# Kernel tuning notes

Measured on AMD Instinct MI355X. Metric: run time of the kernel, lower is better.

The kernel has to match this reference:

```python
import jax, jax.numpy as jnp
import numpy as np

N_EMBD = 1024
N_HEADS = 16
HEAD_DIM = N_EMBD // N_HEADS


def setup_inputs() -> dict:
    key = jax.random.key(0)
    ks = jax.random.split(key, 5)
    s = 0.02
    return {
        "x": jax.random.normal(ks[0], (4, 2048, N_EMBD), dtype=jnp.float32),
        "w_attn": jax.random.normal(ks[1], (N_EMBD, 3 * N_EMBD), dtype=jnp.float32) * s,
        "b_attn": jnp.zeros((3 * N_EMBD,), dtype=jnp.float32),
        "w_proj": jax.random.normal(ks[2], (N_EMBD, N_EMBD), dtype=jnp.float32) * s,
        "b_proj": jnp.zeros((N_EMBD,), dtype=jnp.float32),
    }


def reference(x, w_attn, b_attn, w_proj, b_proj):
    B, T, C = x.shape
    H, D = N_HEADS, HEAD_DIM
    qkv = x @ w_attn + b_attn                      # [B,T,3C]
    q, k, v = jnp.split(qkv, 3, axis=-1)
    q = q.reshape(B, T, H, D).transpose(0, 2, 1, 3)  # [B,H,T,D]
    k = k.reshape(B, T, H, D).transpose(0, 2, 1, 3)
    v = v.reshape(B, T, H, D).transpose(0, 2, 1, 3)
    # Faithful to source bug: divide by d**(-0.5) == multiply by sqrt(d)
    scale = jnp.asarray(D, x.dtype) ** 0.5
    scores = jnp.einsum("bhqd,bhkd->bhqk", q, k) * scale  # [B,H,T,T]
    causal = jnp.tril(jnp.ones((T, T), dtype=bool))
    scores = jnp.where(causal[None, None], scores, -jnp.inf)
    attn = jax.nn.softmax(scores, axis=-1)
    y = jnp.einsum("bhqk,bhkd->bhqd", attn, v)     # [B,H,T,D]
    y = y.transpose(0, 2, 1, 3).reshape(B, T, C)
    return y @ w_proj + b_proj
```

## Files before the change

kernel.cpp:

```cpp
#include <hip/hip_runtime.h>
#include <cmath>

#define BB 4
#define TT 2048
#define CC 1024
#define HH 16
#define DD 64
#define MM (BB*TT)

typedef _Float16 f16x8 __attribute__((ext_vector_type(8)));
typedef float f32x4 __attribute__((ext_vector_type(4)));
typedef unsigned short ushort_t;

__device__ __forceinline__ unsigned short f2h(float f) {
    _Float16 h = (_Float16)f;
    return __builtin_bit_cast(unsigned short, h);
}

__device__ __forceinline__ void gld16(const void* gsrc, void* ldst) {
    void* g = const_cast<void*>(gsrc);
    __builtin_amdgcn_global_load_lds(
        (__attribute__((address_space(1))) void*)g,
        (__attribute__((address_space(3))) void*)ldst,
        16, 0, 0);
}

__global__ __launch_bounds__(256)
void cvt4_kernel(const float* __restrict__ in, ushort_t* __restrict__ out, long n4) {
    long i = (long)blockIdx.x * blockDim.x + threadIdx.x;
    if (i >= n4) return;
    float4 v = ((const float4*)in)[i];
    ushort4 o;
    o.x = f2h(v.x); o.y = f2h(v.y); o.z = f2h(v.z); o.w = f2h(v.w);
    ((ushort4*)out)[i] = o;
}

__global__ __launch_bounds__(256)
void trcvt_kernel(const float* __restrict__ in, ushort_t* __restrict__ out,
                  int K, int N) {
    __shared__ float T[32][33];
    const int tx = threadIdx.x & 31;
    const int ty = threadIdx.x >> 5;
    const int n0 = blockIdx.x * 32;
    const int k0 = blockIdx.y * 32;
    #pragma unroll
    for (int i = 0; i < 4; ++i)
        T[ty + i * 8][tx] = in[(size_t)(k0 + ty + i * 8) * N + n0 + tx];
    __syncthreads();
    #pragma unroll
    for (int i = 0; i < 4; ++i)
        out[(size_t)(n0 + ty + i * 8) * K + k0 + tx] = f2h(T[tx][ty + i * 8]);
}

template<int N, bool QKV>
__global__ __launch_bounds__(256)
void hgemm_kernel(const ushort_t* __restrict__ A, const ushort_t* __restrict__ Bt,
                  const float* __restrict__ bias, float* __restrict__ out,
                  ushort_t* __restrict__ qh, ushort_t* __restrict__ kh,
                  ushort_t* __restrict__ vh)
{
    const int K = 1024;
    __shared__ ushort_t As[128 * 32];
    __shared__ ushort_t Bs[128 * 32];

    const int tid  = threadIdx.x;
    const int lane = tid & 63;
    const int wave = tid >> 6;
    const int wm   = (wave & 1) * 64;
    const int wn   = (wave >> 1) * 64;
    const int m0   = blockIdx.y * 128;
    const int n0   = blockIdx.x * 128;
    const int lrow = lane & 15;
    const int quad = lane >> 4;

    const int u0 = wave * 64 + lane;
    const int u1 = u0 + 256;
    const size_t gA0 = (size_t)(m0 + (u0 >> 2)) * K + (u0 & 3) * 8;
    const size_t gA1 = (size_t)(m0 + (u1 >> 2)) * K + (u1 & 3) * 8;
    const size_t gB0 = (size_t)(n0 + (u0 >> 2)) * K + (u0 & 3) * 8;
    const size_t gB1 = (size_t)(n0 + (u1 >> 2)) * K + (u1 & 3) * 8;
    ushort_t* ldsA0 = &As[(wave * 64) * 8];
    ushort_t* ldsA1 = &As[(256 + wave * 64) * 8];
    ushort_t* ldsB0 = &Bs[(wave * 64) * 8];
    ushort_t* ldsB1 = &Bs[(256 + wave * 64) * 8];

    f32x4 acc[4][4];
    const f32x4 z = {0.f, 0.f, 0.f, 0.f};
    #pragma unroll
    for (int mt = 0; mt < 4; ++mt)
        #pragma unroll
        for (int nt = 0; nt < 4; ++nt)
            acc[mt][nt] = z;

    for (int kk = 0; kk < K; kk += 32) {
        gld16(&A[gA0 + kk],  ldsA0);
        gld16(&A[gA1 + kk],  ldsA1);
        gld16(&Bt[gB0 + kk], ldsB0);
        gld16(&Bt[gB1 + kk], ldsB1);
        __syncthreads();

        f16x8 af[4], bf[4];
        #pragma unroll
        for (int mt = 0; mt < 4; ++mt)
            af[mt] = *(const f16x8*)&As[(wm + mt * 16 + lrow) * 32 + quad * 8];
        #pragma unroll
        for (int nt = 0; nt < 4; ++nt)
            bf[nt] = *(const f16x8*)&Bs[(wn + nt * 16 + lrow) * 32 + quad * 8];
        #pragma unroll
        for (int mt = 0; mt < 4; ++mt)
            #pragma unroll
            for (int nt = 0; nt < 4; ++nt)
                acc[mt][nt] = __builtin_amdgcn_mfma_f32_16x16x32_f16(
                    af[mt], bf[nt], acc[mt][nt], 0, 0, 0);
        __syncthreads();
    }

    #pragma unroll
    for (int mt = 0; mt < 4; ++mt) {
        const int rbase = m0 + wm + mt * 16 + quad * 4;
        #pragma unroll
        for (int nt = 0; nt < 4; ++nt) {
            const int col = n0 + wn + nt * 16 + lrow;
            const float bv = bias[col];
            if (QKV) {
                const int which = col >> 10;
                const int c = col & 1023;
                const int h = c >> 6, d = c & 63;
                const int b = rbase >> 11, t0 = rbase & 2047;
                if (which == 2) {
                    ushort4 pk;
                    pk.x = f2h(acc[mt][nt][0] + bv);
                    pk.y = f2h(acc[mt][nt][1] + bv);
                    pk.z = f2h(acc[mt][nt][2] + bv);
                    pk.w = f2h(acc[mt][nt][3] + bv);
                    *(ushort4*)&vh[(((size_t)b * HH + h) * DD + d) * TT + t0] = pk;
                } else {
                    ushort_t* dst = which ? kh : qh;
                    const float sc = which ? 1.0f : 8.0f;
                    #pragma unroll
                    for (int r = 0; r < 4; ++r)
                        dst[(((size_t)b * HH + h) * TT + t0 + r) * DD + d] =
                            f2h((acc[mt][nt][r] + bv) * sc);
                }
            } else {
                #pragma unroll
                for (int r = 0; r < 4; ++r)
                    out[(size_t)(rbase + r) * N + col] = acc[mt][nt][r] + bv;
            }
        }
    }
}

__global__ __launch_bounds__(256)
void attn_mfma_kernel(const ushort_t* __restrict__ qh, const ushort_t* __restrict__ kh,
                      const ushort_t* __restrict__ vh, ushort_t* __restrict__ yh)
{
    __shared__ ushort_t Ks[64 * 72];
    __shared__ ushort_t Vs[64 * 72];
    __shared__ ushort_t Ps[4][16 * 72];

    const int bh   = blockIdx.x;
    const int qt   = (int)gridDim.y - 1 - (int)blockIdx.y;
    const int tid  = threadIdx.x;
    const int lane = tid & 63;
    const int w    = tid >> 6;
    const int lrow = lane & 15;
    const int quad = lane >> 4;

    const ushort_t* qbase = qh + (size_t)bh * TT * DD;
    const ushort_t* kbase = kh + (size_t)bh * TT * DD;
    const ushort_t* vbase = vh + (size_t)bh * DD * TT;

    const int q0 = qt * 64 + w * 16;
    const f16x8 aq0 = *(const f16x8*)&qbase[(size_t)(q0 + lrow) * DD + quad * 8];
    const f16x8 aq1 = *(const f16x8*)&qbase[(size_t)(q0 + lrow) * DD + 32 + quad * 8];

    const int ur = tid >> 3;
    const int uc = (tid & 7) * 8;

    f32x4 o[4];
    float mi[4], li[4];
    const f32x4 z = {0.f, 0.f, 0.f, 0.f};
    #pragma unroll
    for (int i = 0; i < 4; ++i) { o[i] = z; mi[i] = -1e30f; li[i] = 0.f; }

    for (int kt = 0; kt <= qt; ++kt) {
        uint4 kr0 = *(const uint4*)&kbase[(size_t)(kt * 64 + ur) * DD + uc];
        uint4 kr1 = *(const uint4*)&kbase[(size_t)(kt * 64 + ur + 32) * DD + uc];
        uint4 vr0 = *(const uint4*)&vbase[(size_t)ur * TT + kt * 64 + uc];
        uint4 vr1 = *(const uint4*)&vbase[(size_t)(ur + 32) * TT + kt * 64 + uc];
        __syncthreads();
        *(uint4*)&Ks[(ur)      * 72 + uc] = kr0;
        *(uint4*)&Ks[(ur + 32) * 72 + uc] = kr1;
        *(uint4*)&Vs[(ur)      * 72 + uc] = vr0;
        *(uint4*)&Vs[(ur + 32) * 72 + uc] = vr1;
        __syncthreads();

        f32x4 s[4];
        #pragma unroll
        for (int c = 0; c < 4; ++c) {
            f16x8 b0 = *(const f16x8*)&Ks[(c * 16 + lrow) * 72 + quad * 8];
            f16x8 b1 = *(const f16x8*)&Ks[(c * 16 + lrow) * 72 + 32 + quad * 8];
            s[c] = __builtin_amdgcn_mfma_f32_16x16x32_f16(aq0, b0, z, 0, 0, 0);
            s[c] = __builtin_amdgcn_mfma_f32_16x16x32_f16(aq1, b1, s[c], 0, 0, 0);
        }

        const bool diag = (kt == qt);
        #pragma unroll
        for (int r = 0; r < 4; ++r) {
            if (diag) {
                const int qg = q0 + quad * 4 + r;
                #pragma unroll
                for (int c = 0; c < 4; ++c)
                    if (kt * 64 + c * 16 + lrow > qg) s[c][r] = -1e30f;
            }
            float m = fmaxf(fmaxf(s[0][r], s[1][r]), fmaxf(s[2][r], s[3][r]));
            #pragma unroll
            for (int off = 1; off < 16; off <<= 1)
                m = fmaxf(m, __shfl_xor(m, off, 64));
            const float mnew  = fmaxf(mi[r], m);
            const float alpha = __expf(mi[r] - mnew);
            float rs = 0.f;
            #pragma unroll
            for (int c = 0; c < 4; ++c) {
                const float p = __expf(s[c][r] - mnew);
                rs += p;
                Ps[w][(quad * 4 + r) * 72 + c * 16 + lrow] = f2h(p);
            }
            #pragma unroll
            for (int off = 1; off < 16; off <<= 1)
                rs += __shfl_xor(rs, off, 64);
            li[r] = li[r] * alpha + rs;
            mi[r] = mnew;
            #pragma unroll
            for (int dt = 0; dt < 4; ++dt) o[dt][r] *= alpha;
        }

        f16x8 ap0 = *(const f16x8*)&Ps[w][lrow * 72 + quad * 8];
        f16x8 ap1 = *(const f16x8*)&Ps[w][lrow * 72 + 32 + quad * 8];
        #pragma unroll
        for (int dt = 0; dt < 4; ++dt) {
            f16x8 b0 = *(const f16x8*)&Vs[(dt * 16 + lrow) * 72 + quad * 8];
            f16x8 b1 = *(const f16x8*)&Vs[(dt * 16 + lrow) * 72 + 32 + quad * 8];
            o[dt] = __builtin_amdgcn_mfma_f32_16x16x32_f16(ap0, b0, o[dt], 0, 0, 0);
            o[dt] = __builtin_amdgcn_mfma_f32_16x16x32_f16(ap1, b1, o[dt], 0, 0, 0);
        }
    }

    const int b = bh >> 4, h = bh & 15;
    #pragma unroll
    for (int r = 0; r < 4; ++r) {
        const float inv = 1.0f / li[r];
        const int t = q0 + quad * 4 + r;
        #pragma unroll
        for (int dt = 0; dt < 4; ++dt)
            yh[((size_t)b * TT + t) * CC + h * 64 + dt * 16 + lrow] =
                f2h(o[dt][r] * inv);
    }
}

extern "C" void kernel_launch(void* const* d_in, const int* in_sizes, int n_in,
                              void* d_out, int out_size, void* d_ws, size_t ws_size,
                              hipStream_t stream) {
    const float* x      = (const float*)d_in[0];
    const float* w_attn = (const float*)d_in[1];
    const float* b_attn = (const float*)d_in[2];
    const float* w_proj = (const float*)d_in[3];
    const float* b_proj = (const float*)d_in[4];
    float* out = (float*)d_out;

    const size_t per = (size_t)BB * HH * TT * DD;
    ushort_t* qh  = (ushort_t*)d_ws;
    ushort_t* kh  = qh + per;
    ushort_t* vh  = kh + per;
    ushort_t* xh  = vh + per;
    ushort_t* yh  = xh;
    ushort_t* wat = xh + (size_t)MM * CC;
    ushort_t* wpt = wat + (size_t)3 * CC * CC;

    cvt4_kernel<<<(MM * CC / 4 + 255) / 256, 256, 0, stream>>>(x, xh, MM * CC / 4);
    trcvt_kernel<<<dim3(3 * CC / 32, CC / 32), 256, 0, stream>>>(w_attn, wat, CC, 3 * CC);
    trcvt_kernel<<<dim3(CC / 32, CC / 32), 256, 0, stream>>>(w_proj, wpt, CC, CC);

    hgemm_kernel<3 * CC, true><<<dim3(3 * CC / 128, MM / 128), 256, 0, stream>>>(
        xh, wat, b_attn, nullptr, qh, kh, vh);

    attn_mfma_kernel<<<dim3(BB * HH, TT / 64), 256, 0, stream>>>(qh, kh, vh, yh);

    hgemm_kernel<CC, false><<<dim3(CC / 128, MM / 128), 256, 0, stream>>>(
        yh, wpt, b_proj, out, nullptr, nullptr, nullptr);
}
```

Before: 314.3 us.

## Restructure attention into single-wave blocks with direct K/V register loads and exp2

Attention now runs as 64-thread single-wavefront blocks, each handling 32 query rows as two 16-row sub-tiles. K and V fragments are loaded straight from global memory into registers, which removes the shared-memory staging and both __syncthreads per key tile. The log2(e) factor is folded into the Q scaling so the softmax can use exp2f. The grid is reordered so heavy query tiles launch first. In exchange, K/V reuse across waves now depends on cache hits rather than LDS, and the finer causal tiling changes the load balance.

```diff
diff --git a/kernel.cpp b/kernel.cpp
--- a/kernel.cpp
+++ b/kernel.cpp
@@ -136,7 +136,7 @@
                     *(ushort4*)&vh[(((size_t)b * HH + h) * DD + d) * TT + t0] = pk;
                 } else {
                     ushort_t* dst = which ? kh : qh;
-                    const float sc = which ? 1.0f : 8.0f;
+                    const float sc = which ? 1.0f : 8.0f * 1.44269504088896f;
                     #pragma unroll
                     for (int r = 0; r < 4; ++r)
                         dst[(((size_t)b * HH + h) * TT + t0 + r) * DD + d] =
@@ -151,112 +151,118 @@
     }
 }
 
-__global__ __launch_bounds__(256)
+__global__ __launch_bounds__(64, 3)
 void attn_mfma_kernel(const ushort_t* __restrict__ qh, const ushort_t* __restrict__ kh,
                       const ushort_t* __restrict__ vh, ushort_t* __restrict__ yh)
 {
-    __shared__ ushort_t Ks[64 * 72];
-    __shared__ ushort_t Vs[64 * 72];
-    __shared__ ushort_t Ps[4][16 * 72];
-
-    const int bh   = blockIdx.x;
-    const int qt   = (int)gridDim.y - 1 - (int)blockIdx.y;
-    const int tid  = threadIdx.x;
-    const int lane = tid & 63;
-    const int w    = tid >> 6;
+    __shared__ ushort_t Ps[32 * 68];
+
+    const int qi   = (int)gridDim.x - 1 - (int)blockIdx.x;
+    const int bh   = blockIdx.y;
+    const int lane = threadIdx.x;
     const int lrow = lane & 15;
     const int quad = lane >> 4;
+    const int q0   = qi * 32;
 
     const ushort_t* qbase = qh + (size_t)bh * TT * DD;
     const ushort_t* kbase = kh + (size_t)bh * TT * DD;
     const ushort_t* vbase = vh + (size_t)bh * DD * TT;
 
-    const int q0 = qt * 64 + w * 16;
-    const f16x8 aq0 = *(const f16x8*)&qbase[(size_t)(q0 + lrow) * DD + quad * 8];
-    const f16x8 aq1 = *(const f16x8*)&qbase[(size_t)(q0 + lrow) * DD + 32 + quad * 8];
-
-    const int ur = tid >> 3;
-    const int uc = (tid & 7) * 8;
-
-    f32x4 o[4];
-    float mi[4], li[4];
+    f16x8 aq[2][2];
+    #pragma unroll
+    for (int s = 0; s < 2; ++s) {
+        aq[s][0] = *(const f16x8*)&qbase[(size_t)(q0 + s * 16 + lrow) * DD + quad * 8];
+        aq[s][1] = *(const f16x8*)&qbase[(size_t)(q0 + s * 16 + lrow) * DD + 32 + quad * 8];
+    }
+
+    f32x4 o[2][4];
+    float mi[2][4], li[2][4];
     const f32x4 z = {0.f, 0.f, 0.f, 0.f};
     #pragma unroll
-    for (int i = 0; i < 4; ++i) { o[i] = z; mi[i] = -1e30f; li[i] = 0.f; }
-
-    for (int kt = 0; kt <= qt; ++kt) {
-        uint4 kr0 = *(const uint4*)&kbase[(size_t)(kt * 64 + ur) * DD + uc];
-        uint4 kr1 = *(const uint4*)&kbase[(size_t)(kt * 64 + ur + 32) * DD + uc];
-        uint4 vr0 = *(const uint4*)&vbase[(size_t)ur * TT + kt * 64 + uc];
-        uint4 vr1 = *(const uint4*)&vbase[(size_t)(ur + 32) * TT + kt * 64 + uc];
-        __syncthreads();
-        *(uint4*)&Ks[(ur)      * 72 + uc] = kr0;
-        *(uint4*)&Ks[(ur + 32) * 72 + uc] = kr1;
-        *(uint4*)&Vs[(ur)      * 72 + uc] = vr0;
-        *(uint4*)&Vs[(ur + 32) * 72 + uc] = vr1;
-        __syncthreads();
-
-        f32x4 s[4];
+    for (int s = 0; s < 2; ++s)
+        #pragma unroll
+        for (int i = 0; i < 4; ++i) { o[s][i] = z; mi[s][i] = -1e30f; li[s][i] = 0.f; }
+
+    const int ktmax = (q0 + 31) >> 6;
+    for (int kt = 0; kt <= ktmax; ++kt) {
+        f16x8 kf[4][2], vf[4][2];
         #pragma unroll
         for (int c = 0; c < 4; ++c) {
-            f16x8 b0 = *(const f16x8*)&Ks[(c * 16 + lrow) * 72 + quad * 8];
-            f16x8 b1 = *(const f16x8*)&Ks[(c * 16 + lrow) * 72 + 32 + quad * 8];
-            s[c] = __builtin_amdgcn_mfma_f32_16x16x32_f16(aq0, b0, z, 0, 0, 0);
-            s[c] = __builtin_amdgcn_mfma_f32_16x16x32_f16(aq1, b1, s[c], 0, 0, 0);
-        }
-
-        const bool diag = (kt == qt);
+            const ushort_t* kp = &kbase[(size_t)(kt * 64 + c * 16 + lrow) * DD + quad * 8];
+            kf[c][0] = *(const f16x8*)kp;
+            kf[c][1] = *(const f16x8*)(kp + 32);
+        }
+        #pragma unroll
+        for (int dt = 0; dt < 4; ++dt) {
+            const ushort_t* vp = &vbase[(size_t)(dt * 16 + lrow) * TT + kt * 64 + quad * 8];
+            vf[dt][0] = *(const f16x8*)vp;
+            vf[dt][1] = *(const f16x8*)(vp + 32);
+        }
+
+        const bool diag = (kt == ktmax);
+        #pragma unroll
+        for (int s = 0; s < 2; ++s) {
+            f32x4 sv[4];
+            #pragma unroll
+            for (int c = 0; c < 4; ++c) {
+                sv[c] = __builtin_amdgcn_mfma_f32_16x16x32_f16(aq[s][0], kf[c][0], z, 0, 0, 0);
+                sv[c] = __builtin_amdgcn_mfma_f32_16x16x32_f16(aq[s][1], kf[c][1], sv[c], 0, 0, 0);
+            }
+            #pragma unroll
+            for (int r = 0; r < 4; ++r) {
+                if (diag) {
+                    const int qg = q0 + s * 16 + quad * 4 + r;
+                    #pragma unroll
+                    for (int c = 0; c < 4; ++c)
+                        if (kt * 64 + c * 16 + lrow > qg) sv[c][r] = -3e38f;
+                }
+                float m = fmaxf(fmaxf(sv[0][r], sv[1][r]), fmaxf(sv[2][r], sv[3][r]));
+                #pragma unroll
+                for (int off = 1; off < 16; off <<= 1)
+                    m = fmaxf(m, __shfl_xor(m, off, 64));
+                const float mnew  = fmaxf(mi[s][r], m);
+                const float alpha = exp2f(mi[s][r] - mnew);
+                float rs = 0.f;
+                #pragma unroll
+                for (int c = 0; c < 4; ++c) {
+                    const float p = exp2f(sv[c][r] - mnew);
+                    rs += p;
+                    Ps[(s * 16 + quad * 4 + r) * 68 + c * 16 + lrow] = f2h(p);
+                }
+                #pragma unroll
+                for (int off = 1; off < 16; off <<= 1)
+                    rs += __shfl_xor(rs, off, 64);
+                li[s][r] = li[s][r] * alpha + rs;
+                mi[s][r] = mnew;
+                #pragma unroll
+                for (int dt = 0; dt < 4; ++dt) o[s][dt][r] *= alpha;
+            }
+        }
+
+        #pragma unroll
+        for (int s = 0; s < 2; ++s) {
+            f16x8 ap0 = *(const f16x8*)&Ps[(s * 16 + lrow) * 68 + quad * 8];
+            f16x8 ap1 = *(const f16x8*)&Ps[(s * 16 + lrow) * 68 + 32 + quad * 8];
+            #pragma unroll
+            for (int dt = 0; dt < 4; ++dt) {
+                o[s][dt] = __builtin_amdgcn_mfma_f32_16x16x32_f16(ap0, vf[dt][0], o[s][dt], 0, 0, 0);
+                o[s][dt] = __builtin_amdgcn_mfma_f32_16x16x32_f16(ap1, vf[dt][1], o[s][dt], 0, 0, 0);
+            }
+        }
+    }
+
+    const int b = bh >> 4, h = bh & 15;
+    #pragma unroll
+    for (int s = 0; s < 2; ++s)
         #pragma unroll
         for (int r = 0; r < 4; ++r) {
-            if (diag) {
-                const int qg = q0 + quad * 4 + r;
-                #pragma unroll
-                for (int c = 0; c < 4; ++c)
-                    if (kt * 64 + c * 16 + lrow > qg) s[c][r] = -1e30f;
-            }
-            float m = fmaxf(fmaxf(s[0][r], s[1][r]), fmaxf(s[2][r], s[3][r]));
-            #pragma unroll
-            for (int off = 1; off < 16; off <<= 1)
-                m = fmaxf(m, __shfl_xor(m, off, 64));
-            const float mnew  = fmaxf(mi[r], m);
-            const float alpha = __expf(mi[r] - mnew);
-            float rs = 0.f;
-            #pragma unroll
-            for (int c = 0; c < 4; ++c) {
-                const float p = __expf(s[c][r] - mnew);
-                rs += p;
-                Ps[w][(quad * 4 + r) * 72 + c * 16 + lrow] = f2h(p);
-            }
-            #pragma unroll
-            for (int off = 1; off < 16; off <<= 1)
-                rs += __shfl_xor(rs, off, 64);
-            li[r] = li[r] * alpha + rs;
-            mi[r] = mnew;
-            #pragma unroll
-            for (int dt = 0; dt < 4; ++dt) o[dt][r] *= alpha;
-        }
-
-        f16x8 ap0 = *(const f16x8*)&Ps[w][lrow * 72 + quad * 8];
-        f16x8 ap1 = *(const f16x8*)&Ps[w][lrow * 72 + 32 + quad * 8];
-        #pragma unroll
-        for (int dt = 0; dt < 4; ++dt) {
-            f16x8 b0 = *(const f16x8*)&Vs[(dt * 16 + lrow) * 72 + quad * 8];
-            f16x8 b1 = *(const f16x8*)&Vs[(dt * 16 + lrow) * 72 + 32 + quad * 8];
-            o[dt] = __builtin_amdgcn_mfma_f32_16x16x32_f16(ap0, b0, o[dt], 0, 0, 0);
-            o[dt] = __builtin_amdgcn_mfma_f32_16x16x32_f16(ap1, b1, o[dt], 0, 0, 0);
-        }
-    }
-
-    const int b = bh >> 4, h = bh & 15;
-    #pragma unroll
-    for (int r = 0; r < 4; ++r) {
-        const float inv = 1.0f / li[r];
-        const int t = q0 + quad * 4 + r;
-        #pragma unroll
-        for (int dt = 0; dt < 4; ++dt)
-            yh[((size_t)b * TT + t) * CC + h * 64 + dt * 16 + lrow] =
-                f2h(o[dt][r] * inv);
-    }
+            const float inv = 1.0f / li[s][r];
+            const int t = q0 + s * 16 + quad * 4 + r;
+            #pragma unroll
+            for (int dt = 0; dt < 4; ++dt)
+                yh[((size_t)b * TT + t) * CC + h * 64 + dt * 16 + lrow] =
+                    f2h(o[s][dt][r] * inv);
+        }
 }
 
 extern "C" void kernel_launch(void* const* d_in, const int* in_sizes, int n_in,
@@ -285,7 +291,7 @@
     hgemm_kernel<3 * CC, true><<<dim3(3 * CC / 128, MM / 128), 256, 0, stream>>>(
         xh, wat, b_attn, nullptr, qh, kh, vh);
 
-    attn_mfma_kernel<<<dim3(BB * HH, TT / 64), 256, 0, stream>>>(qh, kh, vh, yh);
+    attn_mfma_kernel<<<dim3(TT / 32, BB * HH), 64, 0, stream>>>(qh, kh, vh, yh);
 
     hgemm_kernel<CC, false><<<dim3(CC / 128, MM / 128), 256, 0, stream>>>(
         yh, wpt, b_proj, out, nullptr, nullptr, nullptr);
```

Result: slower. 412.9 us (+31.4%).

## Pair causal query tiles per block and keep P in registers via transposed MFMA

Applied to the files above, without the earlier changes.

Each attention block now handles two query tiles (qt and 31-qt), so every block does the same amount of causal work and half as many blocks are launched. S is computed transposed (K as the A operand), so the softmax probabilities land directly in the register layout that 16x16x16 MFMA needs for P·V. This removes the LDS round trip for P and most of the cross-lane shuffles. The K/V loads for the next tile are register-prefetched before compute, log2(e) is folded into the Q scale so exp2f can be used, and launch bounds request 4 blocks per SM. The cost is more MFMA instructions of smaller K and higher register pressure.

```diff
diff --git a/kernel.cpp b/kernel.cpp
--- a/kernel.cpp
+++ b/kernel.cpp
@@ -9,8 +9,11 @@
 #define MM (BB*TT)
 
 typedef _Float16 f16x8 __attribute__((ext_vector_type(8)));
+typedef _Float16 f16x4 __attribute__((ext_vector_type(4)));
 typedef float f32x4 __attribute__((ext_vector_type(4)));
 typedef unsigned short ushort_t;
+
+#define MFMA16(a,b,c) __builtin_amdgcn_mfma_f32_16x16x16f16(a,b,c,0,0,0)
 
 __device__ __forceinline__ unsigned short f2h(float f) {
     _Float16 h = (_Float16)f;
@@ -136,7 +139,7 @@
                     *(ushort4*)&vh[(((size_t)b * HH + h) * DD + d) * TT + t0] = pk;
                 } else {
                     ushort_t* dst = which ? kh : qh;
-                    const float sc = which ? 1.0f : 8.0f;
+                    const float sc = which ? 1.0f : 8.0f * 1.44269504088896f;
                     #pragma unroll
                     for (int r = 0; r < 4; ++r)
                         dst[(((size_t)b * HH + h) * TT + t0 + r) * DD + d] =
@@ -151,16 +154,17 @@
     }
 }
 
-__global__ __launch_bounds__(256)
+__global__ __launch_bounds__(256, 4)
 void attn_mfma_kernel(const ushort_t* __restrict__ qh, const ushort_t* __restrict__ kh,
                       const ushort_t* __restrict__ vh, ushort_t* __restrict__ yh)
 {
     __shared__ ushort_t Ks[64 * 72];
     __shared__ ushort_t Vs[64 * 72];
-    __shared__ ushort_t Ps[4][16 * 72];
-
-    const int bh   = blockIdx.x;
-    const int qt   = (int)gridDim.y - 1 - (int)blockIdx.y;
+
+    const int pr   = blockIdx.x;
+    const int bh   = blockIdx.y;
+    const int qtA  = 31 - pr;
+    const int qtB  = pr;
     const int tid  = threadIdx.x;
     const int lane = tid & 63;
     const int w    = tid >> 6;
@@ -170,88 +174,123 @@
     const ushort_t* qbase = qh + (size_t)bh * TT * DD;
     const ushort_t* kbase = kh + (size_t)bh * TT * DD;
     const ushort_t* vbase = vh + (size_t)bh * DD * TT;
-
-    const int q0 = qt * 64 + w * 16;
-    const f16x8 aq0 = *(const f16x8*)&qbase[(size_t)(q0 + lrow) * DD + quad * 8];
-    const f16x8 aq1 = *(const f16x8*)&qbase[(size_t)(q0 + lrow) * DD + 32 + quad * 8];
+    const int b = bh >> 4, h = bh & 15;
 
     const int ur = tid >> 3;
     const int uc = (tid & 7) * 8;
 
-    f32x4 o[4];
-    float mi[4], li[4];
+    int q0w = qtA * 64 + w * 16;
+    f16x8 aq0 = *(const f16x8*)&qbase[(size_t)(q0w + lrow) * DD + quad * 8];
+    f16x8 aq1 = *(const f16x8*)&qbase[(size_t)(q0w + lrow) * DD + 32 + quad * 8];
+
     const f32x4 z = {0.f, 0.f, 0.f, 0.f};
-    #pragma unroll
-    for (int i = 0; i < 4; ++i) { o[i] = z; mi[i] = -1e30f; li[i] = 0.f; }
-
-    for (int kt = 0; kt <= qt; ++kt) {
-        uint4 kr0 = *(const uint4*)&kbase[(size_t)(kt * 64 + ur) * DD + uc];
-        uint4 kr1 = *(const uint4*)&kbase[(size_t)(kt * 64 + ur + 32) * DD + uc];
-        uint4 vr0 = *(const uint4*)&vbase[(size_t)ur * TT + kt * 64 + uc];
-        uint4 vr1 = *(const uint4*)&vbase[(size_t)(ur + 32) * TT + kt * 64 + uc];
+    f32x4 o[4] = {z, z, z, z};
+    float mi = -1e30f, li = 0.f;
+
+    uint4 kr0 = *(const uint4*)&kbase[(size_t)ur * DD + uc];
+    uint4 kr1 = *(const uint4*)&kbase[(size_t)(ur + 32) * DD + uc];
+    uint4 vr0 = *(const uint4*)&vbase[(size_t)ur * TT + uc];
+    uint4 vr1 = *(const uint4*)&vbase[(size_t)(ur + 32) * TT + uc];
+
+    for (int i = 0; i <= 32; ++i) {
+        if (i == qtA + 1) {
+            #pragma unroll
+            for (int r = 0; r < 4; ++r) {
+                const float inv = 1.0f / __shfl(li, quad * 4 + r, 64);
+                const int t = q0w + quad * 4 + r;
+                #pragma unroll
+                for (int dt = 0; dt < 4; ++dt)
+                    yh[((size_t)b * TT + t) * CC + h * 64 + dt * 16 + lrow] =
+                        f2h(o[dt][r] * inv);
+            }
+            q0w = qtB * 64 + w * 16;
+            aq0 = *(const f16x8*)&qbase[(size_t)(q0w + lrow) * DD + quad * 8];
+            aq1 = *(const f16x8*)&qbase[(size_t)(q0w + lrow) * DD + 32 + quad * 8];
+            #pragma unroll
+            for (int dt = 0; dt < 4; ++dt) o[dt] = z;
+            mi = -1e30f; li = 0.f;
+        }
+        const int kt = (i <= qtA) ? i : i - qtA - 1;
+
         __syncthreads();
         *(uint4*)&Ks[(ur)      * 72 + uc] = kr0;
         *(uint4*)&Ks[(ur + 32) * 72 + uc] = kr1;
         *(uint4*)&Vs[(ur)      * 72 + uc] = vr0;
         *(uint4*)&Vs[(ur + 32) * 72 + uc] = vr1;
         __syncthreads();
-
-        f32x4 s[4];
+        if (i < 32) {
+            const int ni  = i + 1;
+            const int nkt = (ni <= qtA) ? ni : ni - qtA - 1;
+            const int nb  = nkt * 64;
+            kr0 = *(const uint4*)&kbase[(size_t)(nb + ur) * DD + uc];
+            kr1 = *(const uint4*)&kbase[(size_t)(nb + ur + 32) * DD + uc];
+            vr0 = *(const uint4*)&vbase[(size_t)ur * TT + nb + uc];
+            vr1 = *(const uint4*)&vbase[(size_t)(ur + 32) * TT + nb + uc];
+        }
+
+        f32x4 sv[4];
         #pragma unroll
         for (int c = 0; c < 4; ++c) {
-            f16x8 b0 = *(const f16x8*)&Ks[(c * 16 + lrow) * 72 + quad * 8];
-            f16x8 b1 = *(const f16x8*)&Ks[(c * 16 + lrow) * 72 + 32 + quad * 8];
-            s[c] = __builtin_amdgcn_mfma_f32_16x16x32_f16(aq0, b0, z, 0, 0, 0);
-            s[c] = __builtin_amdgcn_mfma_f32_16x16x32_f16(aq1, b1, s[c], 0, 0, 0);
-        }
-
-        const bool diag = (kt == qt);
+            f16x8 ka = *(const f16x8*)&Ks[(c * 16 + lrow) * 72 + quad * 8];
+            f16x8 kb = *(const f16x8*)&Ks[(c * 16 + lrow) * 72 + 32 + quad * 8];
+            sv[c] = __builtin_amdgcn_mfma_f32_16x16x32_f16(ka, aq0, z, 0, 0, 0);
+            sv[c] = __builtin_amdgcn_mfma_f32_16x16x32_f16(kb, aq1, sv[c], 0, 0, 0);
+        }
+
+        const int kt2 = kt * 64;
+        const int qg  = q0w + lrow;
+        const bool diag = (i == qtA) || (i == 32);
+        if (diag) {
+            #pragma unroll
+            for (int c = 0; c < 4; ++c)
+                #pragma unroll
+                for (int r = 0; r < 4; ++r)
+                    if (kt2 + c * 16 + quad * 4 + r > qg) sv[c][r] = -3e38f;
+        }
+        float m = -3e38f;
+        #pragma unroll
+        for (int c = 0; c < 4; ++c)
+            #pragma unroll
+            for (int r = 0; r < 4; ++r) m = fmaxf(m, sv[c][r]);
+        m = fmaxf(m, __shfl_xor(m, 16, 64));
+        m = fmaxf(m, __shfl_xor(m, 32, 64));
+        const float mnew  = fmaxf(mi, m);
+        const float alpha = exp2f(mi - mnew);
+        mi = mnew;
+        float rs = 0.f;
+        f16x4 ap[4];
+        #pragma unroll
+        for (int c = 0; c < 4; ++c)
+            #pragma unroll
+            for (int r = 0; r < 4; ++r) {
+                const float p = exp2f(sv[c][r] - mnew);
+                rs += p;
+                ap[c][r] = (_Float16)p;
+            }
+        rs += __shfl_xor(rs, 16, 64);
+        rs += __shfl_xor(rs, 32, 64);
+        li = li * alpha + rs;
+
         #pragma unroll
         for (int r = 0; r < 4; ++r) {
-            if (diag) {
-                const int qg = q0 + quad * 4 + r;
-                #pragma unroll
-                for (int c = 0; c < 4; ++c)
-                    if (kt * 64 + c * 16 + lrow > qg) s[c][r] = -1e30f;
+            const float ar = __shfl(alpha, quad * 4 + r, 64);
+            #pragma unroll
+            for (int dt = 0; dt < 4; ++dt) o[dt][r] *= ar;
+        }
+
+        #pragma unroll
+        for (int dt = 0; dt < 4; ++dt)
+            #pragma unroll
+            for (int c = 0; c < 4; ++c) {
+                f16x4 vb = *(const f16x4*)&Vs[(dt * 16 + lrow) * 72 + c * 16 + quad * 4];
+                o[dt] = MFMA16(ap[c], vb, o[dt]);
             }
-            float m = fmaxf(fmaxf(s[0][r], s[1][r]), fmaxf(s[2][r], s[3][r]));
-            #pragma unroll
-            for (int off = 1; off < 16; off <<= 1)
-                m = fmaxf(m, __shfl_xor(m, off, 64));
-            const float mnew  = fmaxf(mi[r], m);
-            const float alpha = __expf(mi[r] - mnew);
-            float rs = 0.f;
-            #pragma unroll
-            for (int c = 0; c < 4; ++c) {
-                const float p = __expf(s[c][r] - mnew);
-                rs += p;
-                Ps[w][(quad * 4 + r) * 72 + c * 16 + lrow] = f2h(p);
-            }
-            #pragma unroll
-            for (int off = 1; off < 16; off <<= 1)
-                rs += __shfl_xor(rs, off, 64);
-            li[r] = li[r] * alpha + rs;
-            mi[r] = mnew;
-            #pragma unroll
-            for (int dt = 0; dt < 4; ++dt) o[dt][r] *= alpha;
-        }
-
-        f16x8 ap0 = *(const f16x8*)&Ps[w][lrow * 72 + quad * 8];
-        f16x8 ap1 = *(const f16x8*)&Ps[w][lrow * 72 + 32 + quad * 8];
-        #pragma unroll
-        for (int dt = 0; dt < 4; ++dt) {
-            f16x8 b0 = *(const f16x8*)&Vs[(dt * 16 + lrow) * 72 + quad * 8];
-            f16x8 b1 = *(const f16x8*)&Vs[(dt * 16 + lrow) * 72 + 32 + quad * 8];
-            o[dt] = __builtin_amdgcn_mfma_f32_16x16x32_f16(ap0, b0, o[dt], 0, 0, 0);
-            o[dt] = __builtin_amdgcn_mfma_f32_16x16x32_f16(ap1, b1, o[dt], 0, 0, 0);
-        }
     }
 
-    const int b = bh >> 4, h = bh & 15;
     #pragma unroll
     for (int r = 0; r < 4; ++r) {
-        const float inv = 1.0f / li[r];
-        const int t = q0 + quad * 4 + r;
+        const float inv = 1.0f / __shfl(li, quad * 4 + r, 64);
+        const int t = q0w + quad * 4 + r;
         #pragma unroll
         for (int dt = 0; dt < 4; ++dt)
             yh[((size_t)b * TT + t) * CC + h * 64 + dt * 16 + lrow] =
@@ -285,7 +324,7 @@
     hgemm_kernel<3 * CC, true><<<dim3(3 * CC / 128, MM / 128), 256, 0, stream>>>(
         xh, wat, b_attn, nullptr, qh, kh, vh);
 
-    attn_mfma_kernel<<<dim3(BB * HH, TT / 64), 256, 0, stream>>>(qh, kh, vh, yh);
+    attn_mfma_kernel<<<dim3(16, BB * HH), 256, 0, stream>>>(qh, kh, vh, yh);
 
     hgemm_kernel<CC, false><<<dim3(CC / 128, MM / 128), 256, 0, stream>>>(
         yh, wpt, b_proj, out, nullptr, nullptr, nullptr);
```

Result: faster. 282.2 us (-10.2%).
